# Kernel optimization log

Measured on AMD Instinct MI355X. Metric: run time of the kernel, lower is better.

The kernel has to match this reference:

```python
import jax, jax.numpy as jnp
import numpy as np

N = 100000
E = 3200000
K = 10
ALPHA = 0.1
EPS = 1e-5


def setup_inputs() -> dict:
    key = jax.random.key(0)
    ks = jax.random.split(key, 12)
    x = jax.random.normal(ks[0], (N, 512), dtype=jnp.float32)
    edge_index = jax.random.randint(ks[1], (2, E), 0, N, dtype=jnp.int32)
    w1 = jax.random.normal(ks[2], (128, 512), dtype=jnp.float32) * 0.02
    b1 = jnp.zeros((128,), jnp.float32)
    g1 = jnp.ones((128,), jnp.float32)
    be1 = jnp.zeros((128,), jnp.float32)
    m1 = jax.random.normal(ks[3], (128,), dtype=jnp.float32) * 0.1
    v1 = jax.random.uniform(ks[4], (128,), dtype=jnp.float32, minval=0.5, maxval=1.5)
    w2 = jax.random.normal(ks[5], (128, 128), dtype=jnp.float32) * 0.02
    b2 = jnp.zeros((128,), jnp.float32)
    g2 = jnp.ones((128,), jnp.float32)
    be2 = jnp.zeros((128,), jnp.float32)
    m2 = jax.random.normal(ks[6], (128,), dtype=jnp.float32) * 0.1
    v2 = jax.random.uniform(ks[7], (128,), dtype=jnp.float32, minval=0.5, maxval=1.5)
    w3 = jax.random.normal(ks[8], (3, 128), dtype=jnp.float32) * 0.02
    b3 = jnp.zeros((3,), jnp.float32)
    return dict(x=x, edge_index=edge_index, w1=w1, b1=b1, g1=g1, be1=be1, m1=m1, v1=v1,
                w2=w2, b2=b2, g2=g2, be2=be2, m2=m2, v2=v2, w3=w3, b3=b3)


def _bn(y, g, be, m, v):
    return (y - m) * jax.lax.rsqrt(v + EPS) * g + be


def reference(x, edge_index, w1, b1, g1, be1, m1, v1, w2, b2, g2, be2, m2, v2, w3, b3):
    # MLP (eval mode: BN uses running stats, dropout is identity)
    h = jax.nn.relu(_bn(x @ w1.T + b1, g1, be1, m1, v1))
    h = h + jax.nn.relu(_bn(h @ w2.T + b2, g2, be2, m2, v2))
    h = h @ w3.T + b3  # [N, 3]

    # APPNP propagation with GCN normalization + self-loops
    loop = jnp.arange(N, dtype=edge_index.dtype)
    src = jnp.concatenate([edge_index[0], loop])
    dst = jnp.concatenate([edge_index[1], loop])
    deg = jax.ops.segment_sum(jnp.ones_like(src, dtype=h.dtype), dst, num_segments=N)
    dinv = jnp.where(deg > 0, jax.lax.rsqrt(deg), 0.0)
    norm = dinv[src] * dinv[dst]  # [E+N]

    h0 = h
    z = h
    for _ in range(K):
        msg = z[src] * norm[:, None]
        z = jax.ops.segment_sum(msg, dst, num_segments=N)
        z = (1.0 - ALPHA) * z + ALPHA * h0
    return jax.nn.log_softmax(z, axis=1)
```

## Files before the change

### kernel.cpp

```cpp
#include <hip/hip_runtime.h>
#include <cstdint>
#include <cstddef>

#define N_NODES 100000
#define D_IN 512
#define ALPHA 0.1f
#define EPS_BN 1e-5f
#define M_TILE 128
#define BK 64

#define CBITS 8
#define CNODES 256
#define NCBIN 391
#define TILE 8192
#define EPT 32
#define BINCAP 9216

#define NPB 128
#define NB2 782

typedef float f32x4 __attribute__((ext_vector_type(4)));
typedef __bf16 bf16x8 __attribute__((ext_vector_type(8)));
typedef unsigned short u16x8 __attribute__((ext_vector_type(8)));
typedef unsigned short u16x4 __attribute__((ext_vector_type(4)));

__device__ __forceinline__ unsigned short f2bf(float f) {
  unsigned u = __float_as_uint(f);
  u += 0x7fffu + ((u >> 16) & 1u);
  return (unsigned short)(u >> 16);
}
__device__ __forceinline__ float bf2f(unsigned short h) {
  return __uint_as_float(((unsigned)h) << 16);
}

__global__ void k_prep(const float* __restrict__ w1, const float* __restrict__ b1,
                       const float* __restrict__ g1, const float* __restrict__ be1,
                       const float* __restrict__ m1, const float* __restrict__ v1,
                       const float* __restrict__ w2, const float* __restrict__ b2,
                       const float* __restrict__ g2, const float* __restrict__ be2,
                       const float* __restrict__ m2, const float* __restrict__ v2,
                       unsigned short* __restrict__ w1b, unsigned short* __restrict__ w2b,
                       float* __restrict__ bias1, float* __restrict__ bias2,
                       int* __restrict__ bincur) {
  int idx = blockIdx.x * 256 + threadIdx.x;
  if (idx < 65536) {
    int n = idx >> 9;
    float s = g1[n] * rsqrtf(v1[n] + EPS_BN);
    w1b[idx] = f2bf(w1[idx] * s);
  } else if (idx < 81920) {
    int i = idx - 65536;
    int n = i >> 7;
    float s = g2[n] * rsqrtf(v2[n] + EPS_BN);
    w2b[i] = f2bf(w2[i] * s);
  } else if (idx < 82048) {
    int c = idx - 81920;
    float s = g1[c] * rsqrtf(v1[c] + EPS_BN);
    bias1[c] = (b1[c] - m1[c]) * s + be1[c];
  } else if (idx < 82176) {
    int c = idx - 82048;
    float s = g2[c] * rsqrtf(v2[c] + EPS_BN);
    bias2[c] = (b2[c] - m2[c]) * s + be2[c];
  }
  int bi = idx - 82176;
  if (bi >= 0 && bi < NCBIN) bincur[bi] = 0;
}

__global__ void k_scan1(const int* __restrict__ deg, int* __restrict__ bsum) {
  __shared__ int red[256];
  int t = threadIdx.x;
  int i = blockIdx.x * 256 + t;
  red[t] = (i < N_NODES) ? deg[i] : 0;
  __syncthreads();
  for (int off = 128; off > 0; off >>= 1) {
    if (t < off) red[t] += red[t + off];
    __syncthreads();
  }
  if (t == 0) bsum[blockIdx.x] = red[0];
}

#define NB_SCAN 391
__global__ void k_scan2(int* __restrict__ bsum) {
  __shared__ int s[448];
  int t = threadIdx.x;
  for (int i = t; i < 448; i += 256) s[i] = (i < NB_SCAN) ? bsum[i] : 0;
  __syncthreads();
  if (t < 64) {
    int base = t * 7;
    int vals[7];
    int sum = 0;
#pragma unroll
    for (int j = 0; j < 7; ++j) { vals[j] = s[base + j]; sum += vals[j]; }
    int x = sum;
#pragma unroll
    for (int off = 1; off < 64; off <<= 1) {
      int y = __shfl_up(x, off, 64);
      if (t >= off) x += y;
    }
    int run = x - sum;
#pragma unroll
    for (int j = 0; j < 7; ++j) { int tmp = vals[j]; s[base + j] = run; run += tmp; }
  }
  __syncthreads();
  for (int i = t; i < NB_SCAN; i += 256) bsum[i] = s[i];
}

__global__ void k_scan3(const int* __restrict__ deg, const int* __restrict__ bsum,
                        int* __restrict__ row_start, float* __restrict__ dinv, int E) {
  __shared__ int sb[2][256];
  int t = threadIdx.x;
  int i = blockIdx.x * 256 + t;
  int d = (i < N_NODES) ? deg[i] : 0;
  sb[0][t] = d;
  __syncthreads();
  int cur = 0;
#pragma unroll
  for (int off = 1; off < 256; off <<= 1) {
    int val = sb[cur][t] + ((t >= off) ? sb[cur][t - off] : 0);
    sb[cur ^ 1][t] = val;
    __syncthreads();
    cur ^= 1;
  }
  int incl = sb[cur][t];
  int ex = incl - d;
  if (i < N_NODES) {
    int rs = bsum[blockIdx.x] + ex;
    row_start[i] = rs;
    dinv[i] = rsqrtf((float)(d + 1));
  }
  if (i == N_NODES) row_start[N_NODES] = E;
}

__global__ __launch_bounds__(256) void k_binA(const int* __restrict__ src,
                                              const int* __restrict__ dst, int E,
                                              int* __restrict__ bincur,
                                              unsigned* __restrict__ binned) {
  __shared__ unsigned stage[TILE];
  __shared__ int cnt[NCBIN];
  __shared__ int loff[NCBIN + 1];
  __shared__ int goff[NCBIN];
  __shared__ int sc[2][256];
  const int tid = threadIdx.x;

  for (int i = tid; i < NCBIN; i += 256) cnt[i] = 0;
  __syncthreads();

  const int e0 = blockIdx.x * TILE;
  const int n = min(TILE, E - e0);

  unsigned pk[EPT];
  int bp[EPT];
#pragma unroll
  for (int i = 0; i < EPT; ++i) {
    int o = i * 256 + tid;
    if (o < n) {
      int e = e0 + o;
      int d = dst[e];
      int s = src[e];
      int b = d >> CBITS;
      pk[i] = (unsigned)s | ((unsigned)(d & (CNODES - 1)) << 17);
      int p = atomicAdd(&cnt[b], 1);
      bp[i] = b | (p << 9);
    } else bp[i] = -1;
  }
  __syncthreads();

  int c0 = (2 * tid     < NCBIN) ? cnt[2 * tid]     : 0;
  int c1 = (2 * tid + 1 < NCBIN) ? cnt[2 * tid + 1] : 0;
  sc[0][tid] = c0 + c1;
  __syncthreads();
  int cur = 0;
#pragma unroll
  for (int off = 1; off < 256; off <<= 1) {
    sc[cur ^ 1][tid] = sc[cur][tid] + ((tid >= off) ? sc[cur][tid - off] : 0);
    __syncthreads();
    cur ^= 1;
  }
  int ex = sc[cur][tid] - (c0 + c1);
  if (2 * tid < NCBIN) loff[2 * tid] = ex;
  if (2 * tid + 1 < NCBIN) loff[2 * tid + 1] = ex + c0;
  if (tid == 255) loff[NCBIN] = sc[cur][255];
  __syncthreads();
  for (int i = tid; i < NCBIN; i += 256)
    if (cnt[i] > 0) goff[i] = atomicAdd(&bincur[i], cnt[i]);
  __syncthreads();

#pragma unroll
  for (int i = 0; i < EPT; ++i) {
    if (bp[i] >= 0) {
      int b = bp[i] & 511;
      int p = bp[i] >> 9;
      stage[loff[b] + p] = pk[i];
    }
  }
  __syncthreads();

  for (int i = tid; i < n; i += 256) {
    int lo = 0, hi = NCBIN;
    while (hi - lo > 1) { int mid = (lo + hi) >> 1; if (loff[mid] <= i) lo = mid; else hi = mid; }
    int b = lo;
    binned[(size_t)b * BINCAP + goff[b] + (i - loff[b])] = stage[i];
  }
}

__global__ __launch_bounds__(256) void k_binB1(const unsigned* __restrict__ binned,
                                               const int* __restrict__ bincur,
                                               int* __restrict__ deg) {
  __shared__ int lcnt[CNODES];
  int b = blockIdx.x;
  int t = threadIdx.x;
  lcnt[t] = 0;
  __syncthreads();
  int cnt = bincur[b];
  const unsigned* bp = binned + (size_t)b * BINCAP;
  for (int i = t; i < cnt; i += 256) {
    unsigned v = bp[i];
    atomicAdd(&lcnt[v >> 17], 1);
  }
  __syncthreads();
  int node = (b << CBITS) + t;
  if (node < N_NODES) deg[node] = lcnt[t];
}

__global__ __launch_bounds__(256) void k_binB2(const unsigned* __restrict__ binned,
                                               const int* __restrict__ bincur,
                                               const int* __restrict__ row_start,
                                               unsigned* __restrict__ csr_col) {
  __shared__ unsigned sortbuf[BINCAP];
  __shared__ int lcur[CNODES];
  int b = blockIdx.x;
  int t = threadIdx.x;
  int node0 = b << CBITS;
  int nodes = min(CNODES, N_NODES - node0);
  int rs0 = row_start[node0];
  if (t < nodes) lcur[t] = row_start[node0 + t] - rs0;
  __syncthreads();
  int cnt = bincur[b];
  const unsigned* bp = binned + (size_t)b * BINCAP;
  for (int i = t; i < cnt; i += 256) {
    unsigned v = bp[i];
    int p = atomicAdd(&lcur[v >> 17], 1);
    sortbuf[p] = v & 0x1FFFFu;
  }
  __syncthreads();
  for (int i = t; i < cnt; i += 256) csr_col[rs0 + i] = sortbuf[i];
}

__global__ __launch_bounds__(256, 2) void k_mlp(
    const float* __restrict__ x, const unsigned short* __restrict__ w1b,
    const unsigned short* __restrict__ w2b, const float* __restrict__ bias1,
    const float* __restrict__ bias2, const float* __restrict__ w3,
    const float* __restrict__ b3, const float* __restrict__ dinv,
    float4* __restrict__ h0, float4* __restrict__ zt) {
  __shared__ unsigned short arena[35840];
  __shared__ float lds_w3[384];
  unsigned short* lds_x = arena;
  unsigned short* lds_w = arena + 9216;
  unsigned short* lds_h = arena;
  unsigned short* lds_w2 = arena + 18432;

  const int tid = threadIdx.x;
  const int lane = tid & 63;
  const int wv = tid >> 6;
  const int fr = lane & 15;
  const int kq = (lane >> 4) * 8;
  const int rq = (lane >> 4) * 4;
  const int row0 = blockIdx.x * M_TILE;

  for (int i = tid; i < 384; i += 256) lds_w3[i] = w3[i];

#pragma unroll
  for (int it = 0; it < 8; ++it) {
    int idx = it * 256 + tid;
    int n = idx >> 4, c8 = idx & 15;
    uint4 v = *(const uint4*)(w2b + n * 128 + c8 * 8);
    *(uint4*)(lds_w2 + n * 136 + c8 * 8) = v;
  }

  f32x4 zero4 = {0.f, 0.f, 0.f, 0.f};
  f32x4 acc[2][8];
#pragma unroll
  for (int mt = 0; mt < 2; ++mt)
#pragma unroll
    for (int nt = 0; nt < 8; ++nt) acc[mt][nt] = zero4;

  for (int kb = 0; kb < D_IN; kb += BK) {
#pragma unroll
    for (int it = 0; it < 8; ++it) {
      int idx = it * 256 + tid;
      int r = idx >> 4, c4 = idx & 15;
      int gm = row0 + r;
      if (gm >= N_NODES) gm = N_NODES - 1;
      float4 v = *(const float4*)(x + (size_t)gm * D_IN + kb + c4 * 4);
      u16x4 o;
      o.x = f2bf(v.x); o.y = f2bf(v.y); o.z = f2bf(v.z); o.w = f2bf(v.w);
      *(u16x4*)(lds_x + r * 72 + c4 * 4) = o;
    }
#pragma unroll
    for (int it = 0; it < 4; ++it) {
      int idx = it * 256 + tid;
      int n = idx >> 3, c8 = idx & 7;
      uint4 v = *(const uint4*)(w1b + n * 512 + kb + c8 * 8);
      *(uint4*)(lds_w + n * 72 + c8 * 8) = v;
    }
    __syncthreads();
#pragma unroll
    for (int kk = 0; kk < BK; kk += 32) {
      bf16x8 a[2], b[8];
#pragma unroll
      for (int mt = 0; mt < 2; ++mt)
        a[mt] = __builtin_bit_cast(bf16x8, *(const u16x8*)(lds_x + (wv * 32 + mt * 16 + fr) * 72 + kk + kq));
#pragma unroll
      for (int nt = 0; nt < 8; ++nt)
        b[nt] = __builtin_bit_cast(bf16x8, *(const u16x8*)(lds_w + (nt * 16 + fr) * 72 + kk + kq));
#pragma unroll
      for (int mt = 0; mt < 2; ++mt)
#pragma unroll
        for (int nt = 0; nt < 8; ++nt)
          acc[mt][nt] = __builtin_amdgcn_mfma_f32_16x16x32_bf16(a[mt], b[nt], acc[mt][nt], 0, 0, 0);
    }
    __syncthreads();
  }

  float b1v[8], b2v[8];
#pragma unroll
  for (int nt = 0; nt < 8; ++nt) {
    b1v[nt] = bias1[nt * 16 + fr];
    b2v[nt] = bias2[nt * 16 + fr];
  }
  float hr[2][8][4];
#pragma unroll
  for (int mt = 0; mt < 2; ++mt)
#pragma unroll
    for (int nt = 0; nt < 8; ++nt)
#pragma unroll
      for (int r = 0; r < 4; ++r) {
        int rl = wv * 32 + mt * 16 + rq + r;
        int cl = nt * 16 + fr;
        float h = acc[mt][nt][r] + b1v[nt];
        h = h > 0.f ? h : 0.f;
        hr[mt][nt][r] = h;
        lds_h[rl * 136 + cl] = f2bf(h);
      }
  __syncthreads();

  f32x4 acc2[2][8];
#pragma unroll
  for (int mt = 0; mt < 2; ++mt)
#pragma unroll
    for (int nt = 0; nt < 8; ++nt) acc2[mt][nt] = zero4;
#pragma unroll
  for (int kk = 0; kk < 128; kk += 32) {
    bf16x8 a[2], b[8];
#pragma unroll
    for (int mt = 0; mt < 2; ++mt)
      a[mt] = __builtin_bit_cast(bf16x8, *(const u16x8*)(lds_h + (wv * 32 + mt * 16 + fr) * 136 + kk + kq));
#pragma unroll
    for (int nt = 0; nt < 8; ++nt)
      b[nt] = __builtin_bit_cast(bf16x8, *(const u16x8*)(lds_w2 + (nt * 16 + fr) * 136 + kk + kq));
#pragma unroll
    for (int mt = 0; mt < 2; ++mt)
#pragma unroll
      for (int nt = 0; nt < 8; ++nt)
        acc2[mt][nt] = __builtin_amdgcn_mfma_f32_16x16x32_bf16(a[mt], b[nt], acc2[mt][nt], 0, 0, 0);
  }
  __syncthreads();

#pragma unroll
  for (int mt = 0; mt < 2; ++mt)
#pragma unroll
    for (int nt = 0; nt < 8; ++nt)
#pragma unroll
      for (int r = 0; r < 4; ++r) {
        int rl = wv * 32 + mt * 16 + rq + r;
        int cl = nt * 16 + fr;
        float t2 = acc2[mt][nt][r] + b2v[nt];
        t2 = t2 > 0.f ? t2 : 0.f;
        lds_h[rl * 136 + cl] = f2bf(hr[mt][nt][r] + t2);
      }
  __syncthreads();

  if (tid < 128) {
    int m = tid;
    int gm = row0 + m;
    if (gm < N_NODES) {
      float a0 = 0.f, a1 = 0.f, a2 = 0.f;
#pragma unroll 8
      for (int c = 0; c < 128; ++c) {
        float hv = bf2f(lds_h[m * 136 + c]);
        a0 += hv * lds_w3[c];
        a1 += hv * lds_w3[128 + c];
        a2 += hv * lds_w3[256 + c];
      }
      float z0 = a0 + b3[0], z1 = a1 + b3[1], z2 = a2 + b3[2];
      float di = dinv[gm];
      h0[gm] = make_float4(z0, z1, z2, 0.f);
      zt[gm] = make_float4(di * z0, di * z1, di * z2, 0.f);
    }
  }
}

template <bool FINAL>
__global__ __launch_bounds__(256) void k_iter2(
    const float4* __restrict__ zin, float4* __restrict__ zout,
    const int* __restrict__ row_start, const unsigned* __restrict__ csr_col,
    const float* __restrict__ dinv, const float4* __restrict__ h0v,
    float* __restrict__ out) {
  __shared__ float psum[NPB][3];
  const int t = threadIdx.x;
  const int half = t >> 7;
  const int tn = t & 127;
  const int node = blockIdx.x * NPB + tn;
  const bool valid = node < N_NODES;

  int jb = 0, je = 0;
  if (valid) {
    int r0 = row_start[node];
    int r1 = row_start[node + 1];
    int rm = (r0 + r1 + 1) >> 1;
    jb = half ? rm : r0;
    je = half ? r1 : rm;
  }

  float sx = 0.f, sy = 0.f, sz = 0.f;
  int j = jb;
  for (; j + 8 <= je; j += 8) {
    unsigned c0 = csr_col[j + 0], c1 = csr_col[j + 1];
    unsigned c2 = csr_col[j + 2], c3 = csr_col[j + 3];
    unsigned c4 = csr_col[j + 4], c5 = csr_col[j + 5];
    unsigned c6 = csr_col[j + 6], c7 = csr_col[j + 7];
    float4 v0 = zin[c0], v1 = zin[c1], v2 = zin[c2], v3 = zin[c3];
    float4 v4 = zin[c4], v5 = zin[c5], v6 = zin[c6], v7 = zin[c7];
    sx += ((v0.x + v1.x) + (v2.x + v3.x)) + ((v4.x + v5.x) + (v6.x + v7.x));
    sy += ((v0.y + v1.y) + (v2.y + v3.y)) + ((v4.y + v5.y) + (v6.y + v7.y));
    sz += ((v0.z + v1.z) + (v2.z + v3.z)) + ((v4.z + v5.z) + (v6.z + v7.z));
  }
  if (j + 4 <= je) {
    unsigned c0 = csr_col[j + 0], c1 = csr_col[j + 1];
    unsigned c2 = csr_col[j + 2], c3 = csr_col[j + 3];
    float4 v0 = zin[c0], v1 = zin[c1], v2 = zin[c2], v3 = zin[c3];
    sx += (v0.x + v1.x) + (v2.x + v3.x);
    sy += (v0.y + v1.y) + (v2.y + v3.y);
    sz += (v0.z + v1.z) + (v2.z + v3.z);
    j += 4;
  }
  for (; j < je; ++j) {
    float4 v = zin[csr_col[j]];
    sx += v.x; sy += v.y; sz += v.z;
  }

  if (half) { psum[tn][0] = sx; psum[tn][1] = sy; psum[tn][2] = sz; }
  __syncthreads();
  if (half == 0 && valid) {
    float4 self = zin[node];
    float4 h = h0v[node];
    float di = dinv[node];
    sx += psum[tn][0] + self.x;
    sy += psum[tn][1] + self.y;
    sz += psum[tn][2] + self.z;
    float zx = (1.f - ALPHA) * di * sx + ALPHA * h.x;
    float zy = (1.f - ALPHA) * di * sy + ALPHA * h.y;
    float zz = (1.f - ALPHA) * di * sz + ALPHA * h.z;
    if (!FINAL) {
      zout[node] = make_float4(di * zx, di * zy, di * zz, 0.f);
    } else {
      float mx = fmaxf(zx, fmaxf(zy, zz));
      float l = logf(expf(zx - mx) + expf(zy - mx) + expf(zz - mx));
      out[node * 3 + 0] = zx - mx - l;
      out[node * 3 + 1] = zy - mx - l;
      out[node * 3 + 2] = zz - mx - l;
    }
  }
}

extern "C" void kernel_launch(void* const* d_in, const int* in_sizes, int n_in,
                              void* d_out, int out_size, void* d_ws, size_t ws_size,
                              hipStream_t stream) {
  const float* x   = (const float*)d_in[0];
  const int*   ei  = (const int*)d_in[1];
  const float* w1  = (const float*)d_in[2];
  const float* b1  = (const float*)d_in[3];
  const float* g1  = (const float*)d_in[4];
  const float* be1 = (const float*)d_in[5];
  const float* m1  = (const float*)d_in[6];
  const float* v1  = (const float*)d_in[7];
  const float* w2  = (const float*)d_in[8];
  const float* b2  = (const float*)d_in[9];
  const float* g2  = (const float*)d_in[10];
  const float* be2 = (const float*)d_in[11];
  const float* m2  = (const float*)d_in[12];
  const float* v2  = (const float*)d_in[13];
  const float* w3  = (const float*)d_in[14];
  const float* b3  = (const float*)d_in[15];

  const int E = in_sizes[1] / 2;
  const int* srcA = ei;
  const int* dstA = ei + E;

  char* w = (char*)d_ws;
  size_t off = 0;
  auto alloc = [&](size_t bytes) -> void* {
    void* p = w + off;
    off = (off + bytes + 255) & ~(size_t)255;
    return p;
  };
  unsigned short* w1b   = (unsigned short*)alloc(65536 * 2);
  unsigned short* w2b   = (unsigned short*)alloc(16384 * 2);
  float* bias1          = (float*)alloc(128 * 4);
  float* bias2          = (float*)alloc(128 * 4);
  int*   deg            = (int*)alloc((size_t)N_NODES * 4);
  int*   row_start      = (int*)alloc(((size_t)N_NODES + 1) * 4);
  float* dinv           = (float*)alloc((size_t)N_NODES * 4);
  int*   bsum           = (int*)alloc(512 * 4);
  int*   bincur         = (int*)alloc((size_t)NCBIN * 4);
  float4* h0            = (float4*)alloc((size_t)N_NODES * 16);
  float4* ztA           = (float4*)alloc((size_t)N_NODES * 16);
  float4* ztB           = (float4*)alloc((size_t)N_NODES * 16);
  unsigned* csr_col     = (unsigned*)alloc((size_t)E * 4);
  unsigned* binned      = (unsigned*)alloc((size_t)NCBIN * BINCAP * 4);

  const int NB = (N_NODES + 255) / 256;
  const int NTILE = (E + TILE - 1) / TILE;

  k_prep<<<(82176 + NCBIN + 255) / 256, 256, 0, stream>>>(
      w1, b1, g1, be1, m1, v1, w2, b2, g2, be2, m2, v2, w1b, w2b, bias1, bias2, bincur);
  k_binA<<<NTILE, 256, 0, stream>>>(srcA, dstA, E, bincur, binned);
  k_binB1<<<NCBIN, 256, 0, stream>>>(binned, bincur, deg);
  k_scan1<<<NB, 256, 0, stream>>>(deg, bsum);
  k_scan2<<<1, 256, 0, stream>>>(bsum);
  k_scan3<<<NB, 256, 0, stream>>>(deg, bsum, row_start, dinv, E);
  k_binB2<<<NCBIN, 256, 0, stream>>>(binned, bincur, row_start, csr_col);
  k_mlp<<<(N_NODES + M_TILE - 1) / M_TILE, 256, 0, stream>>>(
      x, w1b, w2b, bias1, bias2, w3, b3, dinv, h0, ztA);

  const float4* zin = ztA;
  float4* zout = ztB;
  for (int k = 0; k < 9; ++k) {
    k_iter2<false><<<NB2, 256, 0, stream>>>(zin, zout, row_start, csr_col, dinv, h0, nullptr);
    const float4* tswap = zout;
    zout = (float4*)zin;
    zin = tswap;
  }
  k_iter2<true><<<NB2, 256, 0, stream>>>(zin, nullptr, row_start, csr_col, dinv, h0, (float*)d_out);
}
```

Measured before the change: 628.4 us.

## Split each node's neighbor sum across four threads and drop scan1 pass

The propagation kernel now assigns four threads per node instead of two, with 64 nodes per block and twice as many blocks, and reduces the three partial sums through shared memory. The scalar tail loop becomes fixed 2-wide and 1-wide steps. Separately, the first scan kernel is removed, and the block sums come straight from the per-bin edge counts in bincur, relying on bins of 256 nodes lining up with the 256-node scan blocks. This aims to expose more memory-level parallelism in the gather and cut one launch. In exchange it adds shared-memory reduction work and leaves fewer edges per thread.

```diff
diff --git a/kernel.cpp b/kernel.cpp
--- a/kernel.cpp
+++ b/kernel.cpp
@@ -16,8 +16,8 @@
 #define EPT 32
 #define BINCAP 9216
 
-#define NPB 128
-#define NB2 782
+#define NPB 64
+#define NB2 1563
 
 typedef float f32x4 __attribute__((ext_vector_type(4)));
 typedef __bf16 bf16x8 __attribute__((ext_vector_type(8)));
@@ -65,24 +65,11 @@
   if (bi >= 0 && bi < NCBIN) bincur[bi] = 0;
 }
 
-__global__ void k_scan1(const int* __restrict__ deg, int* __restrict__ bsum) {
-  __shared__ int red[256];
-  int t = threadIdx.x;
-  int i = blockIdx.x * 256 + t;
-  red[t] = (i < N_NODES) ? deg[i] : 0;
-  __syncthreads();
-  for (int off = 128; off > 0; off >>= 1) {
-    if (t < off) red[t] += red[t + off];
-    __syncthreads();
-  }
-  if (t == 0) bsum[blockIdx.x] = red[0];
-}
-
 #define NB_SCAN 391
-__global__ void k_scan2(int* __restrict__ bsum) {
+__global__ void k_scan2(const int* __restrict__ bincur, int* __restrict__ bsum) {
   __shared__ int s[448];
   int t = threadIdx.x;
-  for (int i = t; i < 448; i += 256) s[i] = (i < NB_SCAN) ? bsum[i] : 0;
+  for (int i = t; i < 448; i += 256) s[i] = (i < NB_SCAN) ? bincur[i] : 0;
   __syncthreads();
   if (t < 64) {
     int base = t * 7;
@@ -405,10 +392,10 @@
     const int* __restrict__ row_start, const unsigned* __restrict__ csr_col,
     const float* __restrict__ dinv, const float4* __restrict__ h0v,
     float* __restrict__ out) {
-  __shared__ float psum[NPB][3];
+  __shared__ float psum[3][NPB][3];
   const int t = threadIdx.x;
-  const int half = t >> 7;
-  const int tn = t & 127;
+  const int q = t >> 6;
+  const int tn = t & 63;
   const int node = blockIdx.x * NPB + tn;
   const bool valid = node < N_NODES;
 
@@ -416,9 +403,9 @@
   if (valid) {
     int r0 = row_start[node];
     int r1 = row_start[node + 1];
-    int rm = (r0 + r1 + 1) >> 1;
-    jb = half ? rm : r0;
-    je = half ? r1 : rm;
+    int len = r1 - r0;
+    jb = r0 + ((len * q) >> 2);
+    je = r0 + ((len * (q + 1)) >> 2);
   }
 
   float sx = 0.f, sy = 0.f, sz = 0.f;
@@ -443,20 +430,26 @@
     sz += (v0.z + v1.z) + (v2.z + v3.z);
     j += 4;
   }
-  for (; j < je; ++j) {
+  if (j + 2 <= je) {
+    unsigned c0 = csr_col[j + 0], c1 = csr_col[j + 1];
+    float4 v0 = zin[c0], v1 = zin[c1];
+    sx += v0.x + v1.x; sy += v0.y + v1.y; sz += v0.z + v1.z;
+    j += 2;
+  }
+  if (j < je) {
     float4 v = zin[csr_col[j]];
     sx += v.x; sy += v.y; sz += v.z;
   }
 
-  if (half) { psum[tn][0] = sx; psum[tn][1] = sy; psum[tn][2] = sz; }
-  __syncthreads();
-  if (half == 0 && valid) {
+  if (q) { psum[q - 1][tn][0] = sx; psum[q - 1][tn][1] = sy; psum[q - 1][tn][2] = sz; }
+  __syncthreads();
+  if (q == 0 && valid) {
     float4 self = zin[node];
     float4 h = h0v[node];
     float di = dinv[node];
-    sx += psum[tn][0] + self.x;
-    sy += psum[tn][1] + self.y;
-    sz += psum[tn][2] + self.z;
+    sx += (psum[0][tn][0] + psum[1][tn][0]) + (psum[2][tn][0] + self.x);
+    sy += (psum[0][tn][1] + psum[1][tn][1]) + (psum[2][tn][1] + self.y);
+    sz += (psum[0][tn][2] + psum[1][tn][2]) + (psum[2][tn][2] + self.z);
     float zx = (1.f - ALPHA) * di * sx + ALPHA * h.x;
     float zy = (1.f - ALPHA) * di * sy + ALPHA * h.y;
     float zz = (1.f - ALPHA) * di * sz + ALPHA * h.z;
@@ -525,8 +518,7 @@
       w1, b1, g1, be1, m1, v1, w2, b2, g2, be2, m2, v2, w1b, w2b, bias1, bias2, bincur);
   k_binA<<<NTILE, 256, 0, stream>>>(srcA, dstA, E, bincur, binned);
   k_binB1<<<NCBIN, 256, 0, stream>>>(binned, bincur, deg);
-  k_scan1<<<NB, 256, 0, stream>>>(deg, bsum);
-  k_scan2<<<1, 256, 0, stream>>>(bsum);
+  k_scan2<<<1, 256, 0, stream>>>(bincur, bsum);
   k_scan3<<<NB, 256, 0, stream>>>(deg, bsum, row_start, dinv, E);
   k_binB2<<<NCBIN, 256, 0, stream>>>(binned, bincur, row_start, csr_col);
   k_mlp<<<(N_NODES + M_TILE - 1) / M_TILE, 256, 0, stream>>>(
```

After: 601.3 us. 4.3% less time.
